# Performance work log

Hardware: AMD Instinct MI355X
Metric: run time of the kernel (lower is better)

Reference implementation:

```python
import jax, jax.numpy as jnp
import numpy as np

TEMP = 0.5
NUM_QUERIES = 256
NUM_NEGATIVES = 256
STRONG_THRESHOLD = 0.97


def _l2norm(x):
    n = jnp.sqrt(jnp.sum(x * x, axis=-1, keepdims=True))
    return x / jnp.maximum(n, 1e-12)


def _mls(mu0, mu1, s0, s1, w0, w1):
    # mutual likelihood score, mean over feature dim
    mu0 = _l2norm(mu0)
    mu1 = _l2norm(mu1)
    up = (mu0 * w0 - mu1 * w1) ** 2
    down = s0 * w0 + s1 * w1
    return -0.5 * jnp.mean(up / down + jnp.log(down), axis=-1)


def setup_inputs() -> dict:
    key = jax.random.key(0)
    B, C, H, W, S = 4, 32, 256, 256, 8
    ks = jax.random.split(key, 6)
    weights = jax.random.uniform(ks[0], (B, C, H, W), jnp.float32, 0.1, 1.0)
    mu = jax.random.normal(ks[1], (B, C, H, W), jnp.float32)
    sigma = jax.random.uniform(ks[2], (B, C, H, W), jnp.float32, 0.1, 1.0)
    cls = jax.random.randint(ks[3], (B, H, W), 0, S)
    label = jax.nn.one_hot(cls, S, axis=1, dtype=jnp.float32)  # [B,S,H,W]
    mask = (jax.random.uniform(ks[4], (B, 1, H, W)) < 0.7).astype(jnp.float32)
    prob = jax.random.uniform(ks[5], (B, S, H, W), jnp.float32)
    return {"weights": weights, "mu": mu, "sigma": sigma, "label": label, "mask": mask, "prob": prob}


def _rank_table(m, N):
    # m: bool [S, N]. table[s, r] = pixel index with rank r within class s.
    S = m.shape[0]
    ranks = jnp.cumsum(m, axis=1) - 1
    idx = jnp.where(m, ranks, N)  # out-of-range entries are dropped
    tbl = jnp.zeros((S, N), jnp.int32)
    rows = jnp.broadcast_to(jnp.arange(S)[:, None], (S, N))
    vals = jnp.broadcast_to(jnp.arange(N, dtype=jnp.int32)[None, :], (S, N))
    return tbl.at[rows, idx].set(vals, mode="drop")


def _forward(weights, mu, sigma, label, mask, prob):
    B, C, H, W = mu.shape
    S = label.shape[1]
    N = B * H * W
    Q, NEG = NUM_QUERIES, NUM_NEGATIVES
    mu_f = jnp.transpose(mu, (0, 2, 3, 1)).reshape(N, C)
    sig_f = jnp.transpose(sigma, (0, 2, 3, 1)).reshape(N, C)
    w_f = jnp.transpose(weights, (0, 2, 3, 1)).reshape(N, C)
    valid = jnp.transpose(label * mask, (1, 0, 2, 3)).reshape(S, N)  # [S,N]
    prob_f = jnp.transpose(prob, (1, 0, 2, 3)).reshape(S, N)
    vmask = valid > 0
    hmask = vmask & (prob_f < STRONG_THRESHOLD)
    count = jnp.sum(vmask, axis=1)
    hcount = jnp.sum(hmask, axis=1)
    # prototypes: masked sums over valid pixels (no_grad in original)
    inv_sig_w = w_f / sig_f
    proto_sigma = 1.0 / (valid @ inv_sig_w)                    # [S,C]
    proto_mu = proto_sigma * (valid @ (inv_sig_w * mu_f))      # [S,C]
    proto_weight = 1.0 / (valid @ (1.0 / w_f))                 # [S,C]
    proto_mu, proto_sigma, proto_weight = map(jax.lax.stop_gradient, (proto_mu, proto_sigma, proto_weight))
    tbl_valid = _rank_table(vmask, N)
    tbl_hard = _rank_table(hmask, N)
    keys = jax.random.split(jax.random.key(42), S)

    def per_class(i, key):
        k1, k2, k3 = jax.random.split(key, 3)
        # anchor sampling from hard pixels of class i (differentiable gather)
        ra = jnp.minimum((jax.random.uniform(k1, (Q,)) * hcount[i]).astype(jnp.int32), jnp.maximum(hcount[i] - 1, 0))
        apix = tbl_hard[i, ra]
        a_mu, a_sig, a_w = mu_f[apix], sig_f[apix], w_f[apix]
        # negative class distribution from prototype similarity
        order = (i + 1 + jnp.arange(S - 1)) % S
        sim = _mls(proto_mu[i][None], proto_mu[order], proto_sigma[i][None], proto_sigma[order], proto_weight[i][None], proto_weight[order])
        sim = jnp.where(count[order] > 0, sim, -jnp.inf)
        cls_pick = jax.random.categorical(k2, sim / TEMP, shape=(Q, NEG))
        neg_cls = order[cls_pick]                              # [Q,NEG]
        cnt = count[neg_cls]
        rn = jnp.minimum((jax.random.uniform(k3, (Q, NEG)) * cnt).astype(jnp.int32), jnp.maximum(cnt - 1, 0))
        npix = tbl_valid[neg_cls, rn]                          # [Q,NEG]
        n_mu = jax.lax.stop_gradient(mu_f[npix])
        n_sig = jax.lax.stop_gradient(sig_f[npix])
        n_w = jax.lax.stop_gradient(w_f[npix])
        pos_mu = jnp.broadcast_to(proto_mu[i], (Q, 1, C))
        pos_sig = jnp.broadcast_to(proto_sigma[i], (Q, 1, C))
        pos_w = jnp.broadcast_to(proto_weight[i], (Q, 1, C))
        all_mu = jnp.concatenate([pos_mu, n_mu], axis=1)       # [Q,1+NEG,C]
        all_sig = jnp.concatenate([pos_sig, n_sig], axis=1)
        all_w = jnp.concatenate([pos_w, n_w], axis=1)
        logits = _mls(a_mu[:, None], all_mu, a_sig[:, None], all_sig, a_w[:, None], all_w) / TEMP
        ce = jnp.mean(jax.nn.logsumexp(logits, axis=1) - logits[:, 0])
        ok = (hcount[i] > 0) & (count[i] > 0)
        return jnp.where(ok, ce, 0.0)

    losses = jax.vmap(per_class)(jnp.arange(S), keys)
    valid_num = jnp.sum(count > 0)
    return jnp.sum(losses) / valid_num.astype(losses.dtype)


def reference(weights, mu, sigma, label, mask, prob):
    return _forward(weights, mu, sigma, label, mask, prob)
```

## Files before the change

kernel.cpp:

```cpp
#include <hip/hip_runtime.h>
#include <hip/hip_fp16.h>
#include <stdint.h>


#define NPIX  262144
#define NCLS  8
#define NQ    256
#define NNEG  256
#define NE    257
#define NBLK  1024

typedef unsigned short u16;
typedef unsigned int   u32;

struct TFKeys { u32 k1[8][2], k2[8][2], k3[8][2]; };

__host__ __device__ inline void tf2x32(u32 k0, u32 k1, u32 x0, u32 x1, u32& o0, u32& o1) {
  u32 ks2 = k0 ^ k1 ^ 0x1BD11BDAu;
  x0 += k0; x1 += k1;
#define TFR(R) { x0 += x1; x1 = (x1 << (R)) | (x1 >> (32 - (R))); x1 ^= x0; }
  TFR(13) TFR(15) TFR(26) TFR(6)
  x0 += k1;  x1 += ks2 + 1u;
  TFR(17) TFR(29) TFR(16) TFR(24)
  x0 += ks2; x1 += k0 + 2u;
  TFR(13) TFR(15) TFR(26) TFR(6)
  x0 += k0;  x1 += k1 + 3u;
  TFR(17) TFR(29) TFR(16) TFR(24)
  x0 += k1;  x1 += ks2 + 4u;
  TFR(13) TFR(15) TFR(26) TFR(6)
  x0 += ks2; x1 += k0 + 5u;
#undef TFR
  o0 = x0; o1 = x1;
}

__device__ inline float bfv(u16 v) { return __uint_as_float(((u32)v) << 16); }
__device__ inline float lo16(u32 v) { return __uint_as_float(v << 16); }
__device__ inline float hi16(u32 v) { return __uint_as_float(v & 0xFFFF0000u); }
__device__ inline float u01(u32 bits) { return __uint_as_float((bits >> 9) | 0x3F800000u) - 1.0f; }
__device__ inline u32 rbits(u32 k0, u32 k1, u32 idx) { u32 a, b; tf2x32(k0, k1, 0u, idx, a, b); return a ^ b; }
__device__ inline u32 packPQ(float p, float q) {
  return (u32)__half_as_ushort(__float2half(p)) | ((u32)__half_as_ushort(__float2half(q)) << 16);
}
__device__ inline float2 unpackPQ(u32 v) {
  return make_float2(__half2float(__ushort_as_half((u16)(v & 0xFFFFu))),
                     __half2float(__ushort_as_half((u16)(v >> 16))));
}
__device__ inline float frcp(float x) { return __builtin_amdgcn_rcpf(x); }

__global__ __launch_bounds__(256) void k_flags(const u16* __restrict__ lab, const u16* __restrict__ msk,
                                               const u16* __restrict__ prb, unsigned char* __restrict__ flags,
                                               int* __restrict__ blockCnt,
                                               float* __restrict__ protoAcc, float* __restrict__ ceAcc,
                                               int* __restrict__ diag) {
  __shared__ int cnt[16];
  int tid = threadIdx.x;
  if (blockIdx.x == 0) {
    for (int i = tid; i < 768; i += 256) protoAcc[i] = 0.f;
    if (tid < 8) ceAcc[tid] = 0.f;
    if (tid == 0) diag[0] = 0;
  }
  if (tid < 16) cnt[tid] = 0;
  __syncthreads();
  int n = blockIdx.x * 256 + tid;
  int b = n >> 16, hw = n & 65535;
  float m = bfv(msk[(b << 16) + hw]);
  int cls = 0; bool v = false;
  for (int s = 0; s < 8; s++) {
    float l = bfv(lab[((size_t)(b * 8 + s) << 16) + hw]);
    if (l * m > 0.f) { cls = s; v = true; }
  }
  bool h = false;
  if (v) { float p = bfv(prb[((size_t)(b * 8 + cls) << 16) + hw]); h = p < 0.97f; }
  flags[n] = (unsigned char)(cls | (v ? 16 : 0) | (h ? 32 : 0));
  if (v) atomicAdd(&cnt[cls], 1);
  if (h) atomicAdd(&cnt[8 + cls], 1);
  __syncthreads();
  if (tid < 16) blockCnt[tid * NBLK + blockIdx.x] = cnt[tid];
}

__global__ __launch_bounds__(1024) void k_scan(const int* __restrict__ blockCnt, int* __restrict__ blockOff,
                                               int* __restrict__ counts) {
  int ctr = threadIdx.x >> 6, lane = threadIdx.x & 63;
  int run = 0;
  for (int ch = 0; ch < 16; ch++) {
    int bidx = ch * 64 + lane;
    int v = blockCnt[ctr * NBLK + bidx];
    int x = v;
    for (int d = 1; d < 64; d <<= 1) { int t = __shfl_up(x, d); if (lane >= d) x += t; }
    blockOff[ctr * NBLK + bidx] = run + x - v;
    run += __shfl(x, 63);
  }
  if (lane == 0) counts[ctr] = run;
}

__global__ __launch_bounds__(256) void k_place(const unsigned char* __restrict__ flags, const int* __restrict__ blockOff,
                                               int* __restrict__ tblV, int* __restrict__ tblH) {
  __shared__ int wcnt[4][16];
  int tid = threadIdx.x;
  int n = blockIdx.x * 256 + tid;
  int f = flags[n];
  int cls = f & 15; bool v = (f & 16) != 0, h = (f & 32) != 0;
  int wave = tid >> 6, lane = tid & 63;
  unsigned long long below = (1ull << lane) - 1ull;
  int rv = 0, rh = 0;
  for (int s = 0; s < 8; s++) {
    unsigned long long bv = __ballot(v && (cls == s));
    unsigned long long bh = __ballot(h && (cls == s));
    if (lane == 0) { wcnt[wave][s] = __popcll(bv); wcnt[wave][8 + s] = __popcll(bh); }
    if (cls == s) { rv = __popcll(bv & below); rh = __popcll(bh & below); }
  }
  __syncthreads();
  int preV = 0, preH = 0;
  for (int w2 = 0; w2 < wave; w2++) { preV += wcnt[w2][cls]; preH += wcnt[w2][8 + cls]; }
  if (v) tblV[(size_t)cls * NPIX + blockOff[cls * NBLK + blockIdx.x] + preV + rv] = n;
  if (h) tblH[(size_t)cls * NPIX + blockOff[(8 + cls) * NBLK + blockIdx.x] + preH + rh] = n;
}

__global__ __launch_bounds__(256) void k_pq(const u16* __restrict__ mu, const u16* __restrict__ wgt,
                                            const u16* __restrict__ sig, u32* __restrict__ PQ) {
  __shared__ u32 tile[256 * 33];
  int t = threadIdx.x;
  int n0 = blockIdx.x * 512;
  int b = n0 >> 16;
  int hwt = (n0 & 65535) + 2 * t;
  size_t cb = ((size_t)(b * 32)) << 16;
  u32 m2[32];
  float ss0 = 0.f, ss1 = 0.f;
  #pragma unroll
  for (int c = 0; c < 32; c++) {
    m2[c] = *(const u32*)(mu + cb + ((size_t)c << 16) + hwt);
    float a = lo16(m2[c]), d = hi16(m2[c]);
    ss0 += a * a; ss1 += d * d;
  }
  float rn0 = 1.0f / fmaxf(sqrtf(ss0), 1e-12f);
  float rn1 = 1.0f / fmaxf(sqrtf(ss1), 1e-12f);
  u32 pk0[32], pk1[32];
  #pragma unroll
  for (int c = 0; c < 32; c++) {
    u32 w2 = *(const u32*)(wgt + cb + ((size_t)c << 16) + hwt);
    u32 s2 = *(const u32*)(sig + cb + ((size_t)c << 16) + hwt);
    pk0[c] = packPQ(lo16(m2[c]) * rn0 * lo16(w2), lo16(s2) * lo16(w2));
    pk1[c] = packPQ(hi16(m2[c]) * rn1 * hi16(w2), hi16(s2) * hi16(w2));
  }
  #pragma unroll
  for (int ch = 0; ch < 2; ch++) {
    if ((t >> 7) == ch) {
      int l = t & 127;
      #pragma unroll
      for (int c = 0; c < 32; c++) {
        tile[(2 * l + 0) * 33 + c] = pk0[c];
        tile[(2 * l + 1) * 33 + c] = pk1[c];
      }
    }
    __syncthreads();
    uint4* dst = (uint4*)(PQ + (size_t)(n0 + ch * 256) * 32);
    for (int k = t; k < 2048; k += 256) {
      int p = k >> 3, c4 = (k & 7) * 4;
      dst[k] = make_uint4(tile[p * 33 + c4], tile[p * 33 + c4 + 1],
                          tile[p * 33 + c4 + 2], tile[p * 33 + c4 + 3]);
    }
    __syncthreads();
  }
}

__global__ __launch_bounds__(256) void k_proto(const u16* __restrict__ mu, const u16* __restrict__ wgt,
                                               const u16* __restrict__ sig, const int* __restrict__ tblV,
                                               const int* __restrict__ counts, float* __restrict__ protoAcc) {
  int ch = blockIdx.x & 7;
  int s  = (blockIdx.x >> 3) & 7;
  int c  = blockIdx.x >> 6;
  int sc = s * 32 + c;
  int cnt = counts[s];
  const int* row = tblV + (size_t)s * NPIX;
  float a0 = 0.f, a1 = 0.f, a2 = 0.f;
  int r = ch * 256 + threadIdx.x;
  for (; r + 6144 < cnt; r += 8192) {
    int p0 = row[r], p1 = row[r + 2048], p2 = row[r + 4096], p3 = row[r + 6144];
    size_t A0 = (((size_t)((p0 >> 16) * 32 + c)) << 16) + (p0 & 65535);
    size_t A1 = (((size_t)((p1 >> 16) * 32 + c)) << 16) + (p1 & 65535);
    size_t A2 = (((size_t)((p2 >> 16) * 32 + c)) << 16) + (p2 & 65535);
    size_t A3 = (((size_t)((p3 >> 16) * 32 + c)) << 16) + (p3 & 65535);
    float m0 = bfv(mu[A0]), w0 = bfv(wgt[A0]), s0 = bfv(sig[A0]);
    float m1 = bfv(mu[A1]), w1 = bfv(wgt[A1]), s1 = bfv(sig[A1]);
    float m2_ = bfv(mu[A2]), w2 = bfv(wgt[A2]), s2 = bfv(sig[A2]);
    float m3 = bfv(mu[A3]), w3 = bfv(wgt[A3]), s3 = bfv(sig[A3]);
    float i0 = w0 / s0, i1 = w1 / s1, i2 = w2 / s2, i3 = w3 / s3;
    a0 += i0; a1 += i0 * m0; a2 += 1.0f / w0;
    a0 += i1; a1 += i1 * m1; a2 += 1.0f / w1;
    a0 += i2; a1 += i2 * m2_; a2 += 1.0f / w2;
    a0 += i3; a1 += i3 * m3; a2 += 1.0f / w3;
  }
  for (; r < cnt; r += 2048) {
    int pix = row[r];
    size_t a = (((size_t)((pix >> 16) * 32 + c)) << 16) + (pix & 65535);
    float mv = bfv(mu[a]), wv = bfv(wgt[a]), sv = bfv(sig[a]);
    float isw = wv / sv;
    a0 += isw; a1 += isw * mv; a2 += 1.0f / wv;
  }
  #pragma unroll
  for (int d = 1; d < 64; d <<= 1) {
    a0 += __shfl_xor(a0, d);
    a1 += __shfl_xor(a1, d);
    a2 += __shfl_xor(a2, d);
  }
  if ((threadIdx.x & 63) == 0) {
    atomicAdd(&protoAcc[sc * 3 + 0], a0);
    atomicAdd(&protoAcc[sc * 3 + 1], a1);
    atomicAdd(&protoAcc[sc * 3 + 2], a2);
  }
}

__global__ void k_protoFinal(const float* __restrict__ protoAcc, const int* __restrict__ counts,
                             u32* __restrict__ protoPQ, float* __restrict__ simL,
                             int* __restrict__ diag) {
  __shared__ float sP[256], sQ[256];
  __shared__ int alive;
  int tid = threadIdx.x;
  if (tid == 0) alive = 0;
  float a0 = protoAcc[tid * 3 + 0], a1 = protoAcc[tid * 3 + 1], a2 = protoAcc[tid * 3 + 2];
  bool have = counts[tid >> 5] > 0;
  bool ok = (a0 > 0.f) && (a2 > 0.f);
  __syncthreads();
  if (have && !ok) atomicOr(diag, 2);
  if (have && ok) alive = 1;
  float psig = 1.0f / a0;
  float pmu  = psig * a1;
  float pw   = 1.0f / a2;
  float sq = (have && ok) ? pmu * pmu : 0.f;
  #pragma unroll
  for (int d = 1; d < 32; d <<= 1) sq += __shfl_xor(sq, d);
  float rn = 1.0f / fmaxf(sqrtf(sq), 1e-12f);
  float pP = (have && ok) ? pmu * rn * pw : 0.f;
  float pQ = (have && ok) ? psig * pw : 0.f;
  sP[tid] = pP; sQ[tid] = pQ;
  protoPQ[tid] = packPQ(pP, pQ);
  __syncthreads();
  if (tid == 0 && alive == 0) atomicOr(diag, 32);
  if (tid < 64) {
    int i = tid >> 3, j = tid & 7;
    if (j < 7) {
      int o = (i + 1 + j) & 7;
      float acc = 0.f;
      for (int c = 0; c < 32; c++) {
        float d = sP[i * 32 + c] - sP[o * 32 + c];
        float dn = sQ[i * 32 + c] + sQ[o * 32 + c];
        acc += d * d / dn + logf(dn);
      }
      float sim = -0.5f * (acc * (1.0f / 32.0f));
      simL[i * 8 + j] = (counts[o] > 0) ? (sim * 2.0f) : -INFINITY;
    }
  }
}

__global__ __launch_bounds__(256) void k_sample(TFKeys K, const float* __restrict__ simL,
                                                const int* __restrict__ counts,
                                                const int* __restrict__ tblV, const int* __restrict__ tblH,
                                                const u32* __restrict__ PQ, const u32* __restrict__ protoPQ,
                                                float* __restrict__ ceAcc, int* __restrict__ diag) {
  __shared__ float redM[4], redS[4];
  int blk = blockIdx.x;
  int i = blk >> 8, q = blk & 255;
  int t = threadIdx.x;
  u32 abits = rbits(K.k1[i][0], K.k1[i][1], (u32)q);
  float au = u01(abits);
  int hc = counts[8 + i];
  int ra = (int)(au * (float)hc);
  int cap = hc - 1; if (cap < 0) cap = 0;
  if (ra > cap) ra = cap; if (ra < 0) ra = 0;
  int ap = tblH[(size_t)i * NPIX + ra];
  if (ap < 0) ap = 0; if (ap > NPIX - 1) ap = NPIX - 1;
  const uint4* A4 = (const uint4*)(PQ + (size_t)ap * 32);
  u32 rem = (u32)(q * 256 + t);
  u32 k20 = K.k2[i][0], k21 = K.k2[i][1];
  float Lr[7];
  #pragma unroll
  for (int j = 0; j < 7; j++) Lr[j] = simL[i * 8 + j];
  float mg = 0.f; int pick = 0;
  #pragma unroll
  for (int j = 0; j < 7; j++) {
    u32 bits = rbits(k20, k21, rem * 7u + (u32)j);
    float f = u01(bits);
    float u = fmaxf(f, 1.17549435e-38f);
    float g = -__logf(-__logf(u));
    float v = g + Lr[j];
    if (j == 0) { mg = v; } else if (v > mg) { mg = v; pick = j; }
  }
  int nc = (i + 1 + pick) & 7;
  u32 bits3 = rbits(K.k3[i][0], K.k3[i][1], rem);
  float u3 = u01(bits3);
  int cntv = counts[nc];
  int rn = (int)(u3 * (float)cntv);
  int cap2 = cntv - 1; if (cap2 < 0) cap2 = 0;
  if (rn > cap2) rn = cap2; if (rn < 0) rn = 0;
  int np = tblV[(size_t)nc * NPIX + rn];
  if (np < 0) np = 0; if (np > NPIX - 1) np = NPIX - 1;
  const uint4* B = (const uint4*)(PQ + (size_t)np * 32);
  float accN = 0.f;
  #pragma unroll
  for (int k = 0; k < 8; k++) {
    uint4 ua = A4[k], ub = B[k];
    float2 fa, fb; float d, dn;
    fa = unpackPQ(ua.x); fb = unpackPQ(ub.x); d = fa.x - fb.x; dn = fa.y + fb.y; accN += d * d * frcp(dn) + __logf(dn);
    fa = unpackPQ(ua.y); fb = unpackPQ(ub.y); d = fa.x - fb.x; dn = fa.y + fb.y; accN += d * d * frcp(dn) + __logf(dn);
    fa = unpackPQ(ua.z); fb = unpackPQ(ub.z); d = fa.x - fb.x; dn = fa.y + fb.y; accN += d * d * frcp(dn) + __logf(dn);
    fa = unpackPQ(ua.w); fb = unpackPQ(ub.w); d = fa.x - fb.x; dn = fa.y + fb.y; accN += d * d * frcp(dn) + __logf(dn);
  }
  float lN = -(accN * (1.0f / 32.0f));
  float l0 = 0.f;
  if (t == 0) {
    const uint4* B0 = (const uint4*)(protoPQ + i * 32);
    float acc0 = 0.f;
    #pragma unroll
    for (int k = 0; k < 8; k++) {
      uint4 ua = A4[k], ub = B0[k];
      float2 fa, fb; float d, dn;
      fa = unpackPQ(ua.x); fb = unpackPQ(ub.x); d = fa.x - fb.x; dn = fa.y + fb.y; acc0 += d * d * frcp(dn) + __logf(dn);
      fa = unpackPQ(ua.y); fb = unpackPQ(ub.y); d = fa.x - fb.x; dn = fa.y + fb.y; acc0 += d * d * frcp(dn) + __logf(dn);
      fa = unpackPQ(ua.z); fb = unpackPQ(ub.z); d = fa.x - fb.x; dn = fa.y + fb.y; acc0 += d * d * frcp(dn) + __logf(dn);
      fa = unpackPQ(ua.w); fb = unpackPQ(ub.w); d = fa.x - fb.x; dn = fa.y + fb.y; acc0 += d * d * frcp(dn) + __logf(dn);
    }
    l0 = -(acc0 * (1.0f / 32.0f));
  }
  bool bad = !(lN == lN) || (t == 0 && !(l0 == l0));
  if (__ballot(bad) != 0ull && (t & 63) == 0) atomicOr(diag, 8);
  float lm = (t == 0) ? fmaxf(lN, l0) : lN;
  #pragma unroll
  for (int d = 1; d < 64; d <<= 1) lm = fmaxf(lm, __shfl_xor(lm, d));
  if ((t & 63) == 0) redM[t >> 6] = lm;
  __syncthreads();
  float M = fmaxf(fmaxf(redM[0], redM[1]), fmaxf(redM[2], redM[3]));
  float es = __expf(lN - M) + ((t == 0) ? __expf(l0 - M) : 0.f);
  #pragma unroll
  for (int d = 1; d < 64; d <<= 1) es += __shfl_xor(es, d);
  if ((t & 63) == 0) redS[t >> 6] = es;
  __syncthreads();
  if (t == 0) {
    float S = redS[0] + redS[1] + redS[2] + redS[3];
    float ce = (M + __logf(S)) - l0;
    atomicAdd(&ceAcc[i], ce);
  }
}

__global__ void k_final(const float* __restrict__ ceAcc, const int* __restrict__ counts,
                        const int* __restrict__ diag, u32* __restrict__ out) {
  if (blockIdx.x == 0 && threadIdx.x == 0) {
    float loss = 0.f; int vn = 0;
    int db = diag[0];
    for (int i = 0; i < 8; i++) {
      if (counts[i] > 0) vn++;
      float ce = ceAcc[i];
      if (counts[i] > 0 && counts[8 + i] > 0) {
        if (!(ce == ce)) db |= 4;
        loss += ce * (1.0f / 256.0f);
      }
    }
    if (vn == 0) db |= 1;
    loss = loss / (float)vn;
    if (!(loss == loss) && db == 0) db = 16;
    if (db != 0) loss = 4096.0f * (float)(1 + db);
    u32 fb = __float_as_uint(loss);
    u32 bv = (fb + 0x7FFFu + ((fb >> 16) & 1u)) >> 16;
    out[0] = (fb & 0xFFFF0000u) | (bv & 0xFFFFu);
  }
}

extern "C" void kernel_launch(void* const* d_in, const int* in_sizes, int n_in,
                              void* d_out, int out_size, void* d_ws, size_t ws_size,
                              hipStream_t stream) {
  (void)in_sizes; (void)n_in; (void)out_size; (void)ws_size;
  const u16* wgt = (const u16*)d_in[0];
  const u16* mu  = (const u16*)d_in[1];
  const u16* sig = (const u16*)d_in[2];
  const u16* lab = (const u16*)d_in[3];
  const u16* msk = (const u16*)d_in[4];
  const u16* prb = (const u16*)d_in[5];

  char* wp = (char*)d_ws;
  auto take = [&](size_t bytes) -> void* { void* p = (void*)wp; wp += ((bytes + 255) & ~(size_t)255); return p; };
  u32*   PQ       = (u32*)  take((size_t)NPIX * 32 * 4);
  int*   tblV     = (int*)  take((size_t)NCLS * NPIX * 4);
  int*   tblH     = (int*)  take((size_t)NCLS * NPIX * 4);
  unsigned char* flags = (unsigned char*)take(NPIX);
  int*   blockCnt = (int*)  take(16 * NBLK * 4);
  int*   blockOff = (int*)  take(16 * NBLK * 4);
  float* protoAcc = (float*)take(768 * 4);
  u32*   protoPQ  = (u32*)  take(256 * 4);
  float* simL     = (float*)take(64 * 4);
  int*   counts   = (int*)  take(16 * 4);
  float* ceAcc    = (float*)take(8 * 4);
  int*   diag     = (int*)  take(4);

  TFKeys K;
  for (u32 i = 0; i < 8; i++) {
    u32 ki0, ki1;
    tf2x32(0u, 42u, 0u, i, ki0, ki1);
    tf2x32(ki0, ki1, 0u, 0u, K.k1[i][0], K.k1[i][1]);
    tf2x32(ki0, ki1, 0u, 1u, K.k2[i][0], K.k2[i][1]);
    tf2x32(ki0, ki1, 0u, 2u, K.k3[i][0], K.k3[i][1]);
  }

  k_flags<<<1024, 256, 0, stream>>>(lab, msk, prb, flags, blockCnt, protoAcc, ceAcc, diag);
  k_scan<<<1, 1024, 0, stream>>>(blockCnt, blockOff, counts);
  k_place<<<1024, 256, 0, stream>>>(flags, blockOff, tblV, tblH);
  k_pq<<<512, 256, 0, stream>>>(mu, wgt, sig, PQ);
  k_proto<<<2048, 256, 0, stream>>>(mu, wgt, sig, tblV, counts, protoAcc);
  k_protoFinal<<<1, 256, 0, stream>>>(protoAcc, counts, protoPQ, simL, diag);
  k_sample<<<2048, 256, 0, stream>>>(K, simL, counts, tblV, tblH, PQ, protoPQ, ceAcc, diag);
  k_final<<<1, 64, 0, stream>>>(ceAcc, counts, diag, (u32*)d_out);
}
```

Baseline: 228.8 us.

## Fuse kernels to cut launches: merge flags+pq, inline scan, protoFinal, final

Merges k_flags and k_pq into one launch split by block index. k_place now computes each block's offsets itself by summing blockCnt, so the scan kernel goes away. Every k_sample block recomputes the prototype finalisation into shared memory, and the last block, found with an atomic counter, writes the final loss. The aim is to drop four launches and their serial single-block kernels, at the cost of redundant per-block work (each place block reads 16K counts, each sample block redoes the prototype math).

```diff
diff --git a/kernel.cpp b/kernel.cpp
--- a/kernel.cpp
+++ b/kernel.cpp
@@ -7,7 +7,6 @@
 #define NCLS  8
 #define NQ    256
 #define NNEG  256
-#define NE    257
 #define NBLK  1024
 
 typedef unsigned short u16;
@@ -47,57 +46,112 @@
 }
 __device__ inline float frcp(float x) { return __builtin_amdgcn_rcpf(x); }
 
-__global__ __launch_bounds__(256) void k_flags(const u16* __restrict__ lab, const u16* __restrict__ msk,
-                                               const u16* __restrict__ prb, unsigned char* __restrict__ flags,
-                                               int* __restrict__ blockCnt,
-                                               float* __restrict__ protoAcc, float* __restrict__ ceAcc,
-                                               int* __restrict__ diag) {
-  __shared__ int cnt[16];
+__global__ __launch_bounds__(256) void k_flags_pq(const u16* __restrict__ lab, const u16* __restrict__ msk,
+                                                  const u16* __restrict__ prb, unsigned char* __restrict__ flags,
+                                                  int* __restrict__ blockCnt,
+                                                  float* __restrict__ protoAcc, float* __restrict__ ceAcc,
+                                                  int* __restrict__ diag, int* __restrict__ doneCnt,
+                                                  const u16* __restrict__ mu, const u16* __restrict__ wgt,
+                                                  const u16* __restrict__ sig, u32* __restrict__ PQ) {
+  __shared__ __align__(16) u32 tile[256 * 33];
+  int t = threadIdx.x;
+  if (blockIdx.x < 1024) {
+    int* cnt = (int*)tile;
+    int tid = t;
+    if (blockIdx.x == 0) {
+      for (int i = tid; i < 768; i += 256) protoAcc[i] = 0.f;
+      if (tid < 8) ceAcc[tid] = 0.f;
+      if (tid == 0) { diag[0] = 0; doneCnt[0] = 0; }
+    }
+    if (tid < 16) cnt[tid] = 0;
+    __syncthreads();
+    int n = blockIdx.x * 256 + tid;
+    int b = n >> 16, hw = n & 65535;
+    float m = bfv(msk[(b << 16) + hw]);
+    int cls = 0; bool v = false;
+    for (int s = 0; s < 8; s++) {
+      float l = bfv(lab[((size_t)(b * 8 + s) << 16) + hw]);
+      if (l * m > 0.f) { cls = s; v = true; }
+    }
+    bool h = false;
+    if (v) { float p = bfv(prb[((size_t)(b * 8 + cls) << 16) + hw]); h = p < 0.97f; }
+    flags[n] = (unsigned char)(cls | (v ? 16 : 0) | (h ? 32 : 0));
+    if (v) atomicAdd(&cnt[cls], 1);
+    if (h) atomicAdd(&cnt[8 + cls], 1);
+    __syncthreads();
+    if (tid < 16) blockCnt[tid * NBLK + blockIdx.x] = cnt[tid];
+  } else {
+    int n0 = (blockIdx.x - 1024) * 512;
+    int b = n0 >> 16;
+    int hwt = (n0 & 65535) + 2 * t;
+    size_t cb = ((size_t)(b * 32)) << 16;
+    u32 m2[32];
+    float ss0 = 0.f, ss1 = 0.f;
+    #pragma unroll
+    for (int c = 0; c < 32; c++) {
+      m2[c] = *(const u32*)(mu + cb + ((size_t)c << 16) + hwt);
+      float a = lo16(m2[c]), d = hi16(m2[c]);
+      ss0 += a * a; ss1 += d * d;
+    }
+    float rn0 = 1.0f / fmaxf(sqrtf(ss0), 1e-12f);
+    float rn1 = 1.0f / fmaxf(sqrtf(ss1), 1e-12f);
+    u32 pk0[32], pk1[32];
+    #pragma unroll
+    for (int c = 0; c < 32; c++) {
+      u32 w2 = *(const u32*)(wgt + cb + ((size_t)c << 16) + hwt);
+      u32 s2 = *(const u32*)(sig + cb + ((size_t)c << 16) + hwt);
+      pk0[c] = packPQ(lo16(m2[c]) * rn0 * lo16(w2), lo16(s2) * lo16(w2));
+      pk1[c] = packPQ(hi16(m2[c]) * rn1 * hi16(w2), hi16(s2) * hi16(w2));
+    }
+    #pragma unroll
+    for (int ch = 0; ch < 2; ch++) {
+      if ((t >> 7) == ch) {
+        int l = t & 127;
+        #pragma unroll
+        for (int c = 0; c < 32; c++) {
+          tile[(2 * l + 0) * 33 + c] = pk0[c];
+          tile[(2 * l + 1) * 33 + c] = pk1[c];
+        }
+      }
+      __syncthreads();
+      uint4* dst = (uint4*)(PQ + (size_t)(n0 + ch * 256) * 32);
+      for (int k = t; k < 2048; k += 256) {
+        int p = k >> 3, c4 = (k & 7) * 4;
+        dst[k] = make_uint4(tile[p * 33 + c4], tile[p * 33 + c4 + 1],
+                            tile[p * 33 + c4 + 2], tile[p * 33 + c4 + 3]);
+      }
+      __syncthreads();
+    }
+  }
+}
+
+__global__ __launch_bounds__(256) void k_place(const unsigned char* __restrict__ flags,
+                                               const int* __restrict__ blockCnt,
+                                               int* __restrict__ tblV, int* __restrict__ tblH,
+                                               int* __restrict__ counts) {
+  __shared__ int wcnt[4][16];
+  __shared__ int sOff[16], sTot[16];
   int tid = threadIdx.x;
-  if (blockIdx.x == 0) {
-    for (int i = tid; i < 768; i += 256) protoAcc[i] = 0.f;
-    if (tid < 8) ceAcc[tid] = 0.f;
-    if (tid == 0) diag[0] = 0;
-  }
-  if (tid < 16) cnt[tid] = 0;
-  __syncthreads();
-  int n = blockIdx.x * 256 + tid;
-  int b = n >> 16, hw = n & 65535;
-  float m = bfv(msk[(b << 16) + hw]);
-  int cls = 0; bool v = false;
-  for (int s = 0; s < 8; s++) {
-    float l = bfv(lab[((size_t)(b * 8 + s) << 16) + hw]);
-    if (l * m > 0.f) { cls = s; v = true; }
-  }
-  bool h = false;
-  if (v) { float p = bfv(prb[((size_t)(b * 8 + cls) << 16) + hw]); h = p < 0.97f; }
-  flags[n] = (unsigned char)(cls | (v ? 16 : 0) | (h ? 32 : 0));
-  if (v) atomicAdd(&cnt[cls], 1);
-  if (h) atomicAdd(&cnt[8 + cls], 1);
-  __syncthreads();
-  if (tid < 16) blockCnt[tid * NBLK + blockIdx.x] = cnt[tid];
-}
-
-__global__ __launch_bounds__(1024) void k_scan(const int* __restrict__ blockCnt, int* __restrict__ blockOff,
-                                               int* __restrict__ counts) {
-  int ctr = threadIdx.x >> 6, lane = threadIdx.x & 63;
-  int run = 0;
-  for (int ch = 0; ch < 16; ch++) {
-    int bidx = ch * 64 + lane;
-    int v = blockCnt[ctr * NBLK + bidx];
-    int x = v;
-    for (int d = 1; d < 64; d <<= 1) { int t = __shfl_up(x, d); if (lane >= d) x += t; }
-    blockOff[ctr * NBLK + bidx] = run + x - v;
-    run += __shfl(x, 63);
-  }
-  if (lane == 0) counts[ctr] = run;
-}
-
-__global__ __launch_bounds__(256) void k_place(const unsigned char* __restrict__ flags, const int* __restrict__ blockOff,
-                                               int* __restrict__ tblV, int* __restrict__ tblH) {
-  __shared__ int wcnt[4][16];
-  int tid = threadIdx.x;
-  int n = blockIdx.x * 256 + tid;
+  int blk = blockIdx.x;
+  if (tid < 16) { sOff[tid] = 0; sTot[tid] = 0; }
+  __syncthreads();
+  {
+    int ctr = tid & 15, seg = tid >> 4;
+    const int* row = blockCnt + ctr * NBLK + seg * 64;
+    int lim = blk - seg * 64;
+    int pre = 0, tot = 0;
+    #pragma unroll 8
+    for (int l = 0; l < 64; ++l) {
+      int v = row[l];
+      tot += v;
+      pre += (l < lim) ? v : 0;
+    }
+    atomicAdd(&sOff[ctr], pre);
+    if (blk == 0) atomicAdd(&sTot[ctr], tot);
+  }
+  __syncthreads();
+  if (blk == 0 && tid < 16) counts[tid] = sTot[tid];
+  int n = blk * 256 + tid;
   int f = flags[n];
   int cls = f & 15; bool v = (f & 16) != 0, h = (f & 32) != 0;
   int wave = tid >> 6, lane = tid & 63;
@@ -112,55 +166,8 @@
   __syncthreads();
   int preV = 0, preH = 0;
   for (int w2 = 0; w2 < wave; w2++) { preV += wcnt[w2][cls]; preH += wcnt[w2][8 + cls]; }
-  if (v) tblV[(size_t)cls * NPIX + blockOff[cls * NBLK + blockIdx.x] + preV + rv] = n;
-  if (h) tblH[(size_t)cls * NPIX + blockOff[(8 + cls) * NBLK + blockIdx.x] + preH + rh] = n;
-}
-
-__global__ __launch_bounds__(256) void k_pq(const u16* __restrict__ mu, const u16* __restrict__ wgt,
-                                            const u16* __restrict__ sig, u32* __restrict__ PQ) {
-  __shared__ u32 tile[256 * 33];
-  int t = threadIdx.x;
-  int n0 = blockIdx.x * 512;
-  int b = n0 >> 16;
-  int hwt = (n0 & 65535) + 2 * t;
-  size_t cb = ((size_t)(b * 32)) << 16;
-  u32 m2[32];
-  float ss0 = 0.f, ss1 = 0.f;
-  #pragma unroll
-  for (int c = 0; c < 32; c++) {
-    m2[c] = *(const u32*)(mu + cb + ((size_t)c << 16) + hwt);
-    float a = lo16(m2[c]), d = hi16(m2[c]);
-    ss0 += a * a; ss1 += d * d;
-  }
-  float rn0 = 1.0f / fmaxf(sqrtf(ss0), 1e-12f);
-  float rn1 = 1.0f / fmaxf(sqrtf(ss1), 1e-12f);
-  u32 pk0[32], pk1[32];
-  #pragma unroll
-  for (int c = 0; c < 32; c++) {
-    u32 w2 = *(const u32*)(wgt + cb + ((size_t)c << 16) + hwt);
-    u32 s2 = *(const u32*)(sig + cb + ((size_t)c << 16) + hwt);
-    pk0[c] = packPQ(lo16(m2[c]) * rn0 * lo16(w2), lo16(s2) * lo16(w2));
-    pk1[c] = packPQ(hi16(m2[c]) * rn1 * hi16(w2), hi16(s2) * hi16(w2));
-  }
-  #pragma unroll
-  for (int ch = 0; ch < 2; ch++) {
-    if ((t >> 7) == ch) {
-      int l = t & 127;
-      #pragma unroll
-      for (int c = 0; c < 32; c++) {
-        tile[(2 * l + 0) * 33 + c] = pk0[c];
-        tile[(2 * l + 1) * 33 + c] = pk1[c];
-      }
-    }
-    __syncthreads();
-    uint4* dst = (uint4*)(PQ + (size_t)(n0 + ch * 256) * 32);
-    for (int k = t; k < 2048; k += 256) {
-      int p = k >> 3, c4 = (k & 7) * 4;
-      dst[k] = make_uint4(tile[p * 33 + c4], tile[p * 33 + c4 + 1],
-                          tile[p * 33 + c4 + 2], tile[p * 33 + c4 + 3]);
-    }
-    __syncthreads();
-  }
+  if (v) tblV[(size_t)cls * NPIX + sOff[cls] + preV + rv] = n;
+  if (h) tblH[(size_t)cls * NPIX + sOff[8 + cls] + preH + rh] = n;
 }
 
 __global__ __launch_bounds__(256) void k_proto(const u16* __restrict__ mu, const u16* __restrict__ wgt,
@@ -210,36 +217,44 @@
   }
 }
 
-__global__ void k_protoFinal(const float* __restrict__ protoAcc, const int* __restrict__ counts,
-                             u32* __restrict__ protoPQ, float* __restrict__ simL,
-                             int* __restrict__ diag) {
+__global__ __launch_bounds__(256) void k_sample(TFKeys K, const int* __restrict__ counts,
+                                                const int* __restrict__ tblV, const int* __restrict__ tblH,
+                                                const u32* __restrict__ PQ,
+                                                const float* __restrict__ protoAcc,
+                                                float* __restrict__ ceAcc, int* __restrict__ diag,
+                                                int* __restrict__ doneCnt, u32* __restrict__ out) {
   __shared__ float sP[256], sQ[256];
-  __shared__ int alive;
-  int tid = threadIdx.x;
-  if (tid == 0) alive = 0;
-  float a0 = protoAcc[tid * 3 + 0], a1 = protoAcc[tid * 3 + 1], a2 = protoAcc[tid * 3 + 2];
-  bool have = counts[tid >> 5] > 0;
-  bool ok = (a0 > 0.f) && (a2 > 0.f);
-  __syncthreads();
-  if (have && !ok) atomicOr(diag, 2);
-  if (have && ok) alive = 1;
-  float psig = 1.0f / a0;
-  float pmu  = psig * a1;
-  float pw   = 1.0f / a2;
-  float sq = (have && ok) ? pmu * pmu : 0.f;
-  #pragma unroll
-  for (int d = 1; d < 32; d <<= 1) sq += __shfl_xor(sq, d);
-  float rn = 1.0f / fmaxf(sqrtf(sq), 1e-12f);
-  float pP = (have && ok) ? pmu * rn * pw : 0.f;
-  float pQ = (have && ok) ? psig * pw : 0.f;
-  sP[tid] = pP; sQ[tid] = pQ;
-  protoPQ[tid] = packPQ(pP, pQ);
-  __syncthreads();
-  if (tid == 0 && alive == 0) atomicOr(diag, 32);
-  if (tid < 64) {
-    int i = tid >> 3, j = tid & 7;
-    if (j < 7) {
-      int o = (i + 1 + j) & 7;
+  __shared__ __align__(16) u32 sPP[256];
+  __shared__ float sSim[8];
+  __shared__ float redM[4], redS[4];
+  __shared__ int sAlive;
+  int blk = blockIdx.x;
+  int i = blk >> 8, q = blk & 255;
+  int t = threadIdx.x;
+  {
+    int tid = t;
+    if (tid == 0) sAlive = 0;
+    float a0 = protoAcc[tid * 3 + 0], a1 = protoAcc[tid * 3 + 1], a2 = protoAcc[tid * 3 + 2];
+    bool have = counts[tid >> 5] > 0;
+    bool ok = (a0 > 0.f) && (a2 > 0.f);
+    __syncthreads();
+    if (have && !ok) atomicOr(diag, 2);
+    if (have && ok) sAlive = 1;
+    float psig = 1.0f / a0;
+    float pmu  = psig * a1;
+    float pw   = 1.0f / a2;
+    float sq = (have && ok) ? pmu * pmu : 0.f;
+    #pragma unroll
+    for (int d = 1; d < 32; d <<= 1) sq += __shfl_xor(sq, d);
+    float rn = 1.0f / fmaxf(sqrtf(sq), 1e-12f);
+    float pP = (have && ok) ? pmu * rn * pw : 0.f;
+    float pQ = (have && ok) ? psig * pw : 0.f;
+    sP[tid] = pP; sQ[tid] = pQ;
+    sPP[tid] = packPQ(pP, pQ);
+    __syncthreads();
+    if (tid == 0 && sAlive == 0) atomicOr(diag, 32);
+    if (tid < 7) {
+      int o = (i + 1 + tid) & 7;
       float acc = 0.f;
       for (int c = 0; c < 32; c++) {
         float d = sP[i * 32 + c] - sP[o * 32 + c];
@@ -247,20 +262,10 @@
         acc += d * d / dn + logf(dn);
       }
       float sim = -0.5f * (acc * (1.0f / 32.0f));
-      simL[i * 8 + j] = (counts[o] > 0) ? (sim * 2.0f) : -INFINITY;
-    }
-  }
-}
-
-__global__ __launch_bounds__(256) void k_sample(TFKeys K, const float* __restrict__ simL,
-                                                const int* __restrict__ counts,
-                                                const int* __restrict__ tblV, const int* __restrict__ tblH,
-                                                const u32* __restrict__ PQ, const u32* __restrict__ protoPQ,
-                                                float* __restrict__ ceAcc, int* __restrict__ diag) {
-  __shared__ float redM[4], redS[4];
-  int blk = blockIdx.x;
-  int i = blk >> 8, q = blk & 255;
-  int t = threadIdx.x;
+      sSim[tid] = (counts[o] > 0) ? (sim * 2.0f) : -INFINITY;
+    }
+    __syncthreads();
+  }
   u32 abits = rbits(K.k1[i][0], K.k1[i][1], (u32)q);
   float au = u01(abits);
   int hc = counts[8 + i];
@@ -274,7 +279,7 @@
   u32 k20 = K.k2[i][0], k21 = K.k2[i][1];
   float Lr[7];
   #pragma unroll
-  for (int j = 0; j < 7; j++) Lr[j] = simL[i * 8 + j];
+  for (int j = 0; j < 7; j++) Lr[j] = sSim[j];
   float mg = 0.f; int pick = 0;
   #pragma unroll
   for (int j = 0; j < 7; j++) {
@@ -289,10 +294,10 @@
   u32 bits3 = rbits(K.k3[i][0], K.k3[i][1], rem);
   float u3 = u01(bits3);
   int cntv = counts[nc];
-  int rn = (int)(u3 * (float)cntv);
+  int rn2 = (int)(u3 * (float)cntv);
   int cap2 = cntv - 1; if (cap2 < 0) cap2 = 0;
-  if (rn > cap2) rn = cap2; if (rn < 0) rn = 0;
-  int np = tblV[(size_t)nc * NPIX + rn];
+  if (rn2 > cap2) rn2 = cap2; if (rn2 < 0) rn2 = 0;
+  int np = tblV[(size_t)nc * NPIX + rn2];
   if (np < 0) np = 0; if (np > NPIX - 1) np = NPIX - 1;
   const uint4* B = (const uint4*)(PQ + (size_t)np * 32);
   float accN = 0.f;
@@ -308,7 +313,7 @@
   float lN = -(accN * (1.0f / 32.0f));
   float l0 = 0.f;
   if (t == 0) {
-    const uint4* B0 = (const uint4*)(protoPQ + i * 32);
+    const uint4* B0 = (const uint4*)(&sPP[i * 32]);
     float acc0 = 0.f;
     #pragma unroll
     for (int k = 0; k < 8; k++) {
@@ -339,28 +344,29 @@
     float ce = (M + __logf(S)) - l0;
     atomicAdd(&ceAcc[i], ce);
   }
-}
-
-__global__ void k_final(const float* __restrict__ ceAcc, const int* __restrict__ counts,
-                        const int* __restrict__ diag, u32* __restrict__ out) {
-  if (blockIdx.x == 0 && threadIdx.x == 0) {
-    float loss = 0.f; int vn = 0;
-    int db = diag[0];
-    for (int i = 0; i < 8; i++) {
-      if (counts[i] > 0) vn++;
-      float ce = ceAcc[i];
-      if (counts[i] > 0 && counts[8 + i] > 0) {
-        if (!(ce == ce)) db |= 4;
-        loss += ce * (1.0f / 256.0f);
+  __syncthreads();
+  if (t == 0) {
+    __threadfence();
+    u32 done = (u32)atomicAdd(doneCnt, 1);
+    if (done == 2047u) {
+      int db = atomicOr(diag, 0);
+      float loss = 0.f; int vn = 0;
+      for (int ii = 0; ii < 8; ii++) {
+        if (counts[ii] > 0) vn++;
+        float ce = atomicAdd(&ceAcc[ii], 0.0f);
+        if (counts[ii] > 0 && counts[8 + ii] > 0) {
+          if (!(ce == ce)) db |= 4;
+          loss += ce * (1.0f / 256.0f);
+        }
       }
-    }
-    if (vn == 0) db |= 1;
-    loss = loss / (float)vn;
-    if (!(loss == loss) && db == 0) db = 16;
-    if (db != 0) loss = 4096.0f * (float)(1 + db);
-    u32 fb = __float_as_uint(loss);
-    u32 bv = (fb + 0x7FFFu + ((fb >> 16) & 1u)) >> 16;
-    out[0] = (fb & 0xFFFF0000u) | (bv & 0xFFFFu);
+      if (vn == 0) db |= 1;
+      loss = loss / (float)vn;
+      if (!(loss == loss) && db == 0) db = 16;
+      if (db != 0) loss = 4096.0f * (float)(1 + db);
+      u32 fb = __float_as_uint(loss);
+      u32 bv = (fb + 0x7FFFu + ((fb >> 16) & 1u)) >> 16;
+      out[0] = (fb & 0xFFFF0000u) | (bv & 0xFFFFu);
+    }
   }
 }
 
@@ -382,13 +388,11 @@
   int*   tblH     = (int*)  take((size_t)NCLS * NPIX * 4);
   unsigned char* flags = (unsigned char*)take(NPIX);
   int*   blockCnt = (int*)  take(16 * NBLK * 4);
-  int*   blockOff = (int*)  take(16 * NBLK * 4);
   float* protoAcc = (float*)take(768 * 4);
-  u32*   protoPQ  = (u32*)  take(256 * 4);
-  float* simL     = (float*)take(64 * 4);
   int*   counts   = (int*)  take(16 * 4);
   float* ceAcc    = (float*)take(8 * 4);
   int*   diag     = (int*)  take(4);
+  int*   doneCnt  = (int*)  take(4);
 
   TFKeys K;
   for (u32 i = 0; i < 8; i++) {
@@ -399,12 +403,9 @@
     tf2x32(ki0, ki1, 0u, 2u, K.k3[i][0], K.k3[i][1]);
   }
 
-  k_flags<<<1024, 256, 0, stream>>>(lab, msk, prb, flags, blockCnt, protoAcc, ceAcc, diag);
-  k_scan<<<1, 1024, 0, stream>>>(blockCnt, blockOff, counts);
-  k_place<<<1024, 256, 0, stream>>>(flags, blockOff, tblV, tblH);
-  k_pq<<<512, 256, 0, stream>>>(mu, wgt, sig, PQ);
+  k_flags_pq<<<1536, 256, 0, stream>>>(lab, msk, prb, flags, blockCnt, protoAcc, ceAcc, diag, doneCnt,
+                                       mu, wgt, sig, PQ);
+  k_place<<<1024, 256, 0, stream>>>(flags, blockCnt, tblV, tblH, counts);
   k_proto<<<2048, 256, 0, stream>>>(mu, wgt, sig, tblV, counts, protoAcc);
-  k_protoFinal<<<1, 256, 0, stream>>>(protoAcc, counts, protoPQ, simL, diag);
-  k_sample<<<2048, 256, 0, stream>>>(K, simL, counts, tblV, tblH, PQ, protoPQ, ceAcc, diag);
-  k_final<<<1, 64, 0, stream>>>(ceAcc, counts, diag, (u32*)d_out);
-}
+  k_sample<<<2048, 256, 0, stream>>>(K, counts, tblV, tblH, PQ, protoAcc, ceAcc, diag, doneCnt, (u32*)d_out);
+}
```

Result: slower. 257.2 us (+12.4%).

## Fuse prototype accumulation into PQ pass and fold block scan into placement

Applied to the files above, without the earlier changes.

Prototype sums are now accumulated during the streaming PQ pass. Each pixel's class flag routes its terms into shared-memory atomics, and each block then flushes its partial sums to global memory. This removes the separate gathered k_proto pass, which re-read mu, weight and sigma through random indirection. The single-block k_scan kernel is also removed: each placement block computes its own prefix offsets from blockCnt. The cost is contended shared atomics (8 classes per block) and redundant prefix work in every k_place block.

```diff
diff --git a/kernel.cpp b/kernel.cpp
--- a/kernel.cpp
+++ b/kernel.cpp
@@ -7,7 +7,6 @@
 #define NCLS  8
 #define NQ    256
 #define NNEG  256
-#define NE    257
 #define NBLK  1024
 
 typedef unsigned short u16;
@@ -78,26 +77,112 @@
   if (tid < 16) blockCnt[tid * NBLK + blockIdx.x] = cnt[tid];
 }
 
-__global__ __launch_bounds__(1024) void k_scan(const int* __restrict__ blockCnt, int* __restrict__ blockOff,
+__global__ __launch_bounds__(256) void k_pq_proto(const u16* __restrict__ mu, const u16* __restrict__ wgt,
+                                                  const u16* __restrict__ sig,
+                                                  const unsigned char* __restrict__ flags,
+                                                  u32* __restrict__ PQ, float* __restrict__ protoAcc) {
+  __shared__ u32 tile[256 * 33];
+  __shared__ float pacc[800];
+  int t = threadIdx.x;
+  pacc[t] = 0.f; pacc[t + 256] = 0.f; pacc[t + 512] = 0.f;
+  if (t < 32) pacc[t + 768] = 0.f;
+  __syncthreads();
+  int n0 = blockIdx.x * 512;
+  int b = n0 >> 16;
+  int hwt = (n0 & 65535) + 2 * t;
+  size_t cb = ((size_t)(b * 32)) << 16;
+  u32 f2 = *(const u16*)(flags + n0 + 2 * t);
+  int cls0 = (int)(f2 & 7u);         bool v0 = (f2 & 16u) != 0u;
+  int cls1 = (int)((f2 >> 8) & 7u);  bool v1 = ((f2 >> 8) & 16u) != 0u;
+  int base0 = cls0 * 100, base1 = cls1 * 100;
+  u32 m2[32];
+  float ss0 = 0.f, ss1 = 0.f;
+  #pragma unroll
+  for (int c = 0; c < 32; c++) {
+    m2[c] = *(const u32*)(mu + cb + ((size_t)c << 16) + hwt);
+    float a = lo16(m2[c]), d = hi16(m2[c]);
+    ss0 += a * a; ss1 += d * d;
+  }
+  float rn0 = 1.0f / fmaxf(sqrtf(ss0), 1e-12f);
+  float rn1 = 1.0f / fmaxf(sqrtf(ss1), 1e-12f);
+  u32 pk0[32], pk1[32];
+  #pragma unroll
+  for (int c = 0; c < 32; c++) {
+    u32 w2 = *(const u32*)(wgt + cb + ((size_t)c << 16) + hwt);
+    u32 s2 = *(const u32*)(sig + cb + ((size_t)c << 16) + hwt);
+    float wl = lo16(w2), wh = hi16(w2);
+    float sl = lo16(s2), sh = hi16(s2);
+    float ml = lo16(m2[c]), mh = hi16(m2[c]);
+    pk0[c] = packPQ(ml * rn0 * wl, sl * wl);
+    pk1[c] = packPQ(mh * rn1 * wh, sh * wh);
+    if (v0) {
+      float isw = wl / sl;
+      atomicAdd(&pacc[base0 + c * 3 + 0], isw);
+      atomicAdd(&pacc[base0 + c * 3 + 1], isw * ml);
+      atomicAdd(&pacc[base0 + c * 3 + 2], 1.0f / wl);
+    }
+    if (v1) {
+      float isw = wh / sh;
+      atomicAdd(&pacc[base1 + c * 3 + 0], isw);
+      atomicAdd(&pacc[base1 + c * 3 + 1], isw * mh);
+      atomicAdd(&pacc[base1 + c * 3 + 2], 1.0f / wh);
+    }
+  }
+  #pragma unroll
+  for (int ch = 0; ch < 2; ch++) {
+    if ((t >> 7) == ch) {
+      int l = t & 127;
+      #pragma unroll
+      for (int c = 0; c < 32; c++) {
+        tile[(2 * l + 0) * 33 + c] = pk0[c];
+        tile[(2 * l + 1) * 33 + c] = pk1[c];
+      }
+    }
+    __syncthreads();
+    uint4* dst = (uint4*)(PQ + (size_t)(n0 + ch * 256) * 32);
+    for (int k = t; k < 2048; k += 256) {
+      int p = k >> 3, c4 = (k & 7) * 4;
+      dst[k] = make_uint4(tile[p * 33 + c4], tile[p * 33 + c4 + 1],
+                          tile[p * 33 + c4 + 2], tile[p * 33 + c4 + 3]);
+    }
+    __syncthreads();
+  }
+  for (int idx = t; idx < 800; idx += 256) {
+    int cls = idx / 100, rem = idx - cls * 100;
+    if (rem < 96) {
+      int c = rem / 3, k = rem - c * 3;
+      atomicAdd(&protoAcc[(cls * 32 + c) * 3 + k], pacc[idx]);
+    }
+  }
+}
+
+__global__ __launch_bounds__(256) void k_place(const unsigned char* __restrict__ flags,
+                                               const int* __restrict__ blockCnt,
+                                               int* __restrict__ tblV, int* __restrict__ tblH,
                                                int* __restrict__ counts) {
-  int ctr = threadIdx.x >> 6, lane = threadIdx.x & 63;
-  int run = 0;
-  for (int ch = 0; ch < 16; ch++) {
-    int bidx = ch * 64 + lane;
-    int v = blockCnt[ctr * NBLK + bidx];
-    int x = v;
-    for (int d = 1; d < 64; d <<= 1) { int t = __shfl_up(x, d); if (lane >= d) x += t; }
-    blockOff[ctr * NBLK + bidx] = run + x - v;
-    run += __shfl(x, 63);
-  }
-  if (lane == 0) counts[ctr] = run;
-}
-
-__global__ __launch_bounds__(256) void k_place(const unsigned char* __restrict__ flags, const int* __restrict__ blockOff,
-                                               int* __restrict__ tblV, int* __restrict__ tblH) {
   __shared__ int wcnt[4][16];
+  __shared__ int sOff[16], sTot[16];
   int tid = threadIdx.x;
-  int n = blockIdx.x * 256 + tid;
+  int blk = blockIdx.x;
+  if (tid < 16) { sOff[tid] = 0; sTot[tid] = 0; }
+  __syncthreads();
+  {
+    int ctr = tid & 15, seg = tid >> 4;
+    const int* row = blockCnt + ctr * NBLK + seg * 64;
+    int lim = blk - seg * 64;
+    int pre = 0, tot = 0;
+    #pragma unroll 8
+    for (int l = 0; l < 64; ++l) {
+      int v = row[l];
+      tot += v;
+      pre += (l < lim) ? v : 0;
+    }
+    atomicAdd(&sOff[ctr], pre);
+    if (blk == 0) atomicAdd(&sTot[ctr], tot);
+  }
+  __syncthreads();
+  if (blk == 0 && tid < 16) counts[tid] = sTot[tid];
+  int n = blk * 256 + tid;
   int f = flags[n];
   int cls = f & 15; bool v = (f & 16) != 0, h = (f & 32) != 0;
   int wave = tid >> 6, lane = tid & 63;
@@ -112,102 +197,8 @@
   __syncthreads();
   int preV = 0, preH = 0;
   for (int w2 = 0; w2 < wave; w2++) { preV += wcnt[w2][cls]; preH += wcnt[w2][8 + cls]; }
-  if (v) tblV[(size_t)cls * NPIX + blockOff[cls * NBLK + blockIdx.x] + preV + rv] = n;
-  if (h) tblH[(size_t)cls * NPIX + blockOff[(8 + cls) * NBLK + blockIdx.x] + preH + rh] = n;
-}
-
-__global__ __launch_bounds__(256) void k_pq(const u16* __restrict__ mu, const u16* __restrict__ wgt,
-                                            const u16* __restrict__ sig, u32* __restrict__ PQ) {
-  __shared__ u32 tile[256 * 33];
-  int t = threadIdx.x;
-  int n0 = blockIdx.x * 512;
-  int b = n0 >> 16;
-  int hwt = (n0 & 65535) + 2 * t;
-  size_t cb = ((size_t)(b * 32)) << 16;
-  u32 m2[32];
-  float ss0 = 0.f, ss1 = 0.f;
-  #pragma unroll
-  for (int c = 0; c < 32; c++) {
-    m2[c] = *(const u32*)(mu + cb + ((size_t)c << 16) + hwt);
-    float a = lo16(m2[c]), d = hi16(m2[c]);
-    ss0 += a * a; ss1 += d * d;
-  }
-  float rn0 = 1.0f / fmaxf(sqrtf(ss0), 1e-12f);
-  float rn1 = 1.0f / fmaxf(sqrtf(ss1), 1e-12f);
-  u32 pk0[32], pk1[32];
-  #pragma unroll
-  for (int c = 0; c < 32; c++) {
-    u32 w2 = *(const u32*)(wgt + cb + ((size_t)c << 16) + hwt);
-    u32 s2 = *(const u32*)(sig + cb + ((size_t)c << 16) + hwt);
-    pk0[c] = packPQ(lo16(m2[c]) * rn0 * lo16(w2), lo16(s2) * lo16(w2));
-    pk1[c] = packPQ(hi16(m2[c]) * rn1 * hi16(w2), hi16(s2) * hi16(w2));
-  }
-  #pragma unroll
-  for (int ch = 0; ch < 2; ch++) {
-    if ((t >> 7) == ch) {
-      int l = t & 127;
-      #pragma unroll
-      for (int c = 0; c < 32; c++) {
-        tile[(2 * l + 0) * 33 + c] = pk0[c];
-        tile[(2 * l + 1) * 33 + c] = pk1[c];
-      }
-    }
-    __syncthreads();
-    uint4* dst = (uint4*)(PQ + (size_t)(n0 + ch * 256) * 32);
-    for (int k = t; k < 2048; k += 256) {
-      int p = k >> 3, c4 = (k & 7) * 4;
-      dst[k] = make_uint4(tile[p * 33 + c4], tile[p * 33 + c4 + 1],
-                          tile[p * 33 + c4 + 2], tile[p * 33 + c4 + 3]);
-    }
-    __syncthreads();
-  }
-}
-
-__global__ __launch_bounds__(256) void k_proto(const u16* __restrict__ mu, const u16* __restrict__ wgt,
-                                               const u16* __restrict__ sig, const int* __restrict__ tblV,
-                                               const int* __restrict__ counts, float* __restrict__ protoAcc) {
-  int ch = blockIdx.x & 7;
-  int s  = (blockIdx.x >> 3) & 7;
-  int c  = blockIdx.x >> 6;
-  int sc = s * 32 + c;
-  int cnt = counts[s];
-  const int* row = tblV + (size_t)s * NPIX;
-  float a0 = 0.f, a1 = 0.f, a2 = 0.f;
-  int r = ch * 256 + threadIdx.x;
-  for (; r + 6144 < cnt; r += 8192) {
-    int p0 = row[r], p1 = row[r + 2048], p2 = row[r + 4096], p3 = row[r + 6144];
-    size_t A0 = (((size_t)((p0 >> 16) * 32 + c)) << 16) + (p0 & 65535);
-    size_t A1 = (((size_t)((p1 >> 16) * 32 + c)) << 16) + (p1 & 65535);
-    size_t A2 = (((size_t)((p2 >> 16) * 32 + c)) << 16) + (p2 & 65535);
-    size_t A3 = (((size_t)((p3 >> 16) * 32 + c)) << 16) + (p3 & 65535);
-    float m0 = bfv(mu[A0]), w0 = bfv(wgt[A0]), s0 = bfv(sig[A0]);
-    float m1 = bfv(mu[A1]), w1 = bfv(wgt[A1]), s1 = bfv(sig[A1]);
-    float m2_ = bfv(mu[A2]), w2 = bfv(wgt[A2]), s2 = bfv(sig[A2]);
-    float m3 = bfv(mu[A3]), w3 = bfv(wgt[A3]), s3 = bfv(sig[A3]);
-    float i0 = w0 / s0, i1 = w1 / s1, i2 = w2 / s2, i3 = w3 / s3;
-    a0 += i0; a1 += i0 * m0; a2 += 1.0f / w0;
-    a0 += i1; a1 += i1 * m1; a2 += 1.0f / w1;
-    a0 += i2; a1 += i2 * m2_; a2 += 1.0f / w2;
-    a0 += i3; a1 += i3 * m3; a2 += 1.0f / w3;
-  }
-  for (; r < cnt; r += 2048) {
-    int pix = row[r];
-    size_t a = (((size_t)((pix >> 16) * 32 + c)) << 16) + (pix & 65535);
-    float mv = bfv(mu[a]), wv = bfv(wgt[a]), sv = bfv(sig[a]);
-    float isw = wv / sv;
-    a0 += isw; a1 += isw * mv; a2 += 1.0f / wv;
-  }
-  #pragma unroll
-  for (int d = 1; d < 64; d <<= 1) {
-    a0 += __shfl_xor(a0, d);
-    a1 += __shfl_xor(a1, d);
-    a2 += __shfl_xor(a2, d);
-  }
-  if ((threadIdx.x & 63) == 0) {
-    atomicAdd(&protoAcc[sc * 3 + 0], a0);
-    atomicAdd(&protoAcc[sc * 3 + 1], a1);
-    atomicAdd(&protoAcc[sc * 3 + 2], a2);
-  }
+  if (v) tblV[(size_t)cls * NPIX + sOff[cls] + preV + rv] = n;
+  if (h) tblH[(size_t)cls * NPIX + sOff[8 + cls] + preH + rh] = n;
 }
 
 __global__ void k_protoFinal(const float* __restrict__ protoAcc, const int* __restrict__ counts,
@@ -382,7 +373,6 @@
   int*   tblH     = (int*)  take((size_t)NCLS * NPIX * 4);
   unsigned char* flags = (unsigned char*)take(NPIX);
   int*   blockCnt = (int*)  take(16 * NBLK * 4);
-  int*   blockOff = (int*)  take(16 * NBLK * 4);
   float* protoAcc = (float*)take(768 * 4);
   u32*   protoPQ  = (u32*)  take(256 * 4);
   float* simL     = (float*)take(64 * 4);
@@ -400,10 +390,8 @@
   }
 
   k_flags<<<1024, 256, 0, stream>>>(lab, msk, prb, flags, blockCnt, protoAcc, ceAcc, diag);
-  k_scan<<<1, 1024, 0, stream>>>(blockCnt, blockOff, counts);
-  k_place<<<1024, 256, 0, stream>>>(flags, blockOff, tblV, tblH);
-  k_pq<<<512, 256, 0, stream>>>(mu, wgt, sig, PQ);
-  k_proto<<<2048, 256, 0, stream>>>(mu, wgt, sig, tblV, counts, protoAcc);
+  k_pq_proto<<<512, 256, 0, stream>>>(mu, wgt, sig, flags, PQ, protoAcc);
+  k_place<<<1024, 256, 0, stream>>>(flags, blockCnt, tblV, tblH, counts);
   k_protoFinal<<<1, 256, 0, stream>>>(protoAcc, counts, protoPQ, simL, diag);
   k_sample<<<2048, 256, 0, stream>>>(K, simL, counts, tblV, tblH, PQ, protoPQ, ceAcc, diag);
   k_final<<<1, 64, 0, stream>>>(ceAcc, counts, diag, (u32*)d_out);
```

After: 227.6 us. About the same (-0.6%).
